# Performance work log

Hardware: AMD Instinct MI355X
Metric: run time of the kernel (lower is better)

## Reference

```python
import jax, jax.numpy as jnp
import numpy as np

S, B, H, NH, M = 2048, 2, 2048, 16, 2048
D = H // NH
FF = 4 * H
NORM = float(np.sqrt(D))  # norm_factor = sqrt(head_dim), no layer scaling
MASK_FILL = jnp.float32(-1e4)


def _ln(x, g, b):
    mu = jnp.mean(x, -1, keepdims=True)
    var = jnp.mean(jnp.square(x - mu), -1, keepdims=True)
    return (x - mu) * jax.lax.rsqrt(var + 1e-5) * g + b


def _l2(x):  # F.normalize over last dim
    return x * jax.lax.rsqrt(jnp.sum(jnp.square(x), -1, keepdims=True) + 1e-12)


def _mlp(h, w1, b1, w2, b2):  # ParallelMLP: h -> 4h -> h with gelu
    return jax.nn.gelu(h @ w1 + b1) @ w2 + b2


def setup_inputs() -> dict:
    key = jax.random.key(0)
    ks = jax.random.split(key, 12)
    w = lambda k, sh: jax.random.normal(k, sh, jnp.float32) * 0.02
    return {
        'x': jax.random.normal(ks[0], (S, B, H), jnp.float32),
        'mem_hidden': jax.random.normal(ks[1], (M, B, H), jnp.float32),
        'mem_mask': jax.random.randint(ks[2], (B, 1, S, M), 0, 5) == 0,  # True = masked
        'ln1_g': jnp.ones((H,), jnp.float32), 'ln1_b': jnp.zeros((H,), jnp.float32),
        'ln2_g': jnp.ones((H,), jnp.float32), 'ln2_b': jnp.zeros((H,), jnp.float32),
        'ln3_g': jnp.ones((H,), jnp.float32), 'ln3_b': jnp.zeros((H,), jnp.float32),
        'w_mlp1_in': w(ks[3], (H, FF)), 'b_mlp1_in': jnp.zeros((FF,), jnp.float32),
        'w_mlp1_out': w(ks[4], (FF, H)), 'b_mlp1_out': jnp.zeros((H,), jnp.float32),
        'w_q': w(ks[5], (H, H)), 'b_q': jnp.zeros((H,), jnp.float32),
        'w_kv': w(ks[6], (H, 2 * H)), 'b_kv': jnp.zeros((2 * H,), jnp.float32),
        'w_dense': w(ks[7], (H, H)), 'b_dense': jnp.zeros((H,), jnp.float32),
        'w_mlp2_in': w(ks[8], (H, FF)), 'b_mlp2_in': jnp.zeros((FF,), jnp.float32),
        'w_mlp2_out': w(ks[9], (FF, H)), 'b_mlp2_out': jnp.zeros((H,), jnp.float32),
    }


def reference(x, mem_hidden, mem_mask, ln1_g, ln1_b, ln2_g, ln2_b, ln3_g, ln3_b,
              w_mlp1_in, b_mlp1_in, w_mlp1_out, b_mlp1_out,
              w_q, b_q, w_kv, b_kv, w_dense, b_dense,
              w_mlp2_in, b_mlp2_in, w_mlp2_out, b_mlp2_out):
    # NOTE: source literally replaces x with mlp1 output (no residual on mlp1)
    x = _mlp(_ln(x, ln1_g, ln1_b), w_mlp1_in, b_mlp1_in, w_mlp1_out, b_mlp1_out)

    # memory attention: l2-normalized query vs l2-normalized retrieved memory k/v
    h2 = _ln(x, ln2_g, ln2_b)
    q = _l2((h2 @ w_q + b_q).reshape(S, B, NH, D))              # [s,b,h,d]
    kv = (mem_hidden @ w_kv + b_kv).reshape(M, B, NH, 2 * D)    # hidden_to_kv
    k = _l2(kv[..., :D])                                        # [m,b,h,d]
    v = _l2(kv[..., D:])
    scores = jnp.einsum('sbhd,mbhd->bhsm', q, k) / NORM
    scores = jnp.where(mem_mask, MASK_FILL, scores)             # attention_mask_func fill
    probs = jax.nn.softmax(scores, axis=-1)
    ctx = jnp.einsum('bhsm,mbhd->sbhd', probs, v).reshape(S, B, H)
    x = x + ctx @ w_dense + b_dense                             # dense w/ skip_bias_add

    x = x + _mlp(_ln(x, ln3_g, ln3_b), w_mlp2_in, b_mlp2_in, w_mlp2_out, b_mlp2_out)
    return x
```

## Files before the change

### kernel.cpp

```cpp
#include <hip/hip_runtime.h>
#include <stdint.h>
#include <stddef.h>

typedef __attribute__((ext_vector_type(8))) short bf16x8;
typedef __attribute__((ext_vector_type(4))) float f32x4;
typedef unsigned short u16;
typedef unsigned int u32;

static constexpr int S_ = 2048, B_ = 2, H_ = 2048, NH_ = 16, D_ = 128, M_ = 2048, FF_ = 8192;
static constexpr int SB_ = S_ * B_;
static constexpr int MB_ = M_ * B_;

__device__ __forceinline__ float b2f(u16 b) {
  union { u32 u; float f; } v; v.u = ((u32)b) << 16; return v.f;
}
__device__ __forceinline__ u16 f2b(float f) {
  union { float f; u32 u; } v; v.f = f;
  u32 u = v.u;
  return (u16)((u + 0x7FFFu + ((u >> 16) & 1u)) >> 16);
}
__device__ __forceinline__ float geluf(float x) {
  float x3 = x * x * x;
  return 0.5f * x * (1.0f + tanhf(0.7978845608028654f * (x + 0.044715f * x3)));
}

#define LDSP(p) (reinterpret_cast<__attribute__((address_space(3))) uint32_t*>(reinterpret_cast<uintptr_t>(p)))
#define GLBP(p) (reinterpret_cast<const __attribute__((address_space(1))) uint32_t*>(reinterpret_cast<uintptr_t>(p)))

__global__ void detect_kinds(const u32* __restrict__ x0, const u32* __restrict__ mask, int* __restrict__ flags) {
  if (threadIdx.x == 0 && blockIdx.x == 0) {
    int cnt = 0;
    for (int i = 0; i < 256; ++i) {
      u32 e = (x0[i] >> 7) & 0xFFu;
      if (e >= 118u && e <= 130u) ++cnt;
    }
    flags[0] = (cnt >= 128) ? 0 : 1;
    int all01 = 1, allf = 1, allb = 1;
    for (int i = 0; i < 256; ++i) {
      u32 v = mask[i];
      if (v > 1u) all01 = 0;
      if (v != 0u && v != 0x3F800000u) allf = 0;
      u32 lo = v & 0xFFFFu, hi = v >> 16;
      if ((lo != 0u && lo != 0x3F80u) || (hi != 0u && hi != 0x3F80u)) allb = 0;
    }
    flags[1] = all01 ? 1 : (allf ? 3 : (allb ? 2 : 0));
  }
}

__global__ void mask_cvt(const void* __restrict__ mraw, const int* __restrict__ flags, u16* __restrict__ mm) {
  int i = blockIdx.x * 256 + threadIdx.x;
  int kind = flags[1];
  int masked;
  if (kind == 1)      masked = ((const int*)mraw)[i] != 0;
  else if (kind == 3) masked = ((const float*)mraw)[i] != 0.0f;
  else if (kind == 2) masked = ((const u16*)mraw)[i] != 0;
  else                masked = ((const unsigned char*)mraw)[i] != 0;
  mm[i] = masked ? 0 : 0x3F80u;
}

__global__ void cvt_f32(const void* __restrict__ src, const int* __restrict__ flags, float* __restrict__ dst, int n) {
  int i = blockIdx.x * 256 + threadIdx.x;
  if (i < n) dst[i] = flags[0] ? ((const float*)src)[i] : b2f(((const u16*)src)[i]);
}

__global__ void cast_in_bf16(const void* __restrict__ src, const int* __restrict__ flags, u16* __restrict__ dst, int n8) {
  int i = blockIdx.x * 256 + threadIdx.x;
  if (i >= n8) return;
  if (flags[0]) {
    const float4* p = (const float4*)src;
    float4 a = p[i * 2], c = p[i * 2 + 1];
    bf16x8 o;
    o[0] = (short)f2b(a.x); o[1] = (short)f2b(a.y); o[2] = (short)f2b(a.z); o[3] = (short)f2b(a.w);
    o[4] = (short)f2b(c.x); o[5] = (short)f2b(c.y); o[6] = (short)f2b(c.z); o[7] = (short)f2b(c.w);
    *(bf16x8*)&dst[i * 8] = o;
  } else {
    *(bf16x8*)&dst[i * 8] = ((const bf16x8*)src)[i];
  }
}

__global__ __launch_bounds__(256) void transpose_cast(const void* __restrict__ in, const int* __restrict__ flags,
                                                      u16* __restrict__ out, int R, int C) {
  __shared__ u16 tile[64][65];
  const int isf = flags[0];
  const int tr = blockIdx.y * 64, tc = blockIdx.x * 64;
  const int tx = threadIdx.x & 63, ty = threadIdx.x >> 6;
  const float* inf = (const float*)in;
  const u16* inb = (const u16*)in;
#pragma unroll
  for (int i = 0; i < 16; ++i) {
    int r = ty * 16 + i;
    size_t idx = (size_t)(tr + r) * C + tc + tx;
    tile[r][tx] = isf ? f2b(inf[idx]) : inb[idx];
  }
  __syncthreads();
#pragma unroll
  for (int i = 0; i < 16; ++i) {
    int c = ty * 16 + i;
    out[(size_t)(tc + c) * R + tr + tx] = tile[tx][c];
  }
}

template <int EXT>
__global__ __launch_bounds__(256) void layernorm_k(const void* __restrict__ xin, const int* __restrict__ flags,
                                                   const float* __restrict__ g, const float* __restrict__ bta,
                                                   u16* __restrict__ out) {
  const int row = blockIdx.x, t = threadIdx.x;
  float v[8];
  bool bfmode = EXT && (flags[0] == 0);
  if (bfmode) {
    const u16* xr = (const u16*)xin + (size_t)row * H_ + t * 8;
    bf16x8 a = *(const bf16x8*)xr;
#pragma unroll
    for (int j = 0; j < 8; ++j) v[j] = b2f((u16)a[j]);
  } else {
    const float* xr = (const float*)xin + (size_t)row * H_ + t * 8;
    float4 a = *(const float4*)xr, c = *(const float4*)(xr + 4);
    v[0] = a.x; v[1] = a.y; v[2] = a.z; v[3] = a.w;
    v[4] = c.x; v[5] = c.y; v[6] = c.z; v[7] = c.w;
  }
  float s1 = 0.f, s2 = 0.f;
#pragma unroll
  for (int j = 0; j < 8; ++j) { s1 += v[j]; s2 += v[j] * v[j]; }
#pragma unroll
  for (int off = 32; off > 0; off >>= 1) { s1 += __shfl_down(s1, off); s2 += __shfl_down(s2, off); }
  __shared__ float red[8];
  const int w = t >> 6;
  if ((t & 63) == 0) { red[w] = s1; red[4 + w] = s2; }
  __syncthreads();
  s1 = red[0] + red[1] + red[2] + red[3];
  s2 = red[4] + red[5] + red[6] + red[7];
  const float mean = s1 * (1.0f / H_);
  const float rstd = rsqrtf(s2 * (1.0f / H_) - mean * mean + 1e-5f);
  bf16x8 o;
#pragma unroll
  for (int j = 0; j < 8; ++j) {
    float y = (v[j] - mean) * rstd * g[t * 8 + j] + bta[t * 8 + j];
    o[j] = (short)f2b(y);
  }
  *(bf16x8*)(out + (size_t)row * H_ + t * 8) = o;
}

template <int BN, int GELU, int RES, int WF, int WB, int ODYN>
__global__ __launch_bounds__(512, 2) void gemm64(const u16* __restrict__ A, const u16* __restrict__ Bt,
                                                 const float* __restrict__ bias, const float* __restrict__ res,
                                                 void* __restrict__ outF, u16* __restrict__ outB,
                                                 const int* __restrict__ flags, int Mr, int N, int K) {
  constexpr int AF = (BN == 256) ? 8 : 4;
  constexpr int NB = (BN == 256) ? 4 : 2;
  constexpr int BSLOT = BN * 64;
  constexpr int SLOTSTR = 16384 + BSLOT;
  __shared__ u16 lds[2 * SLOTSTR];
  const int t = threadIdx.x;
  const int w = t >> 6, lr = t & 15, lk = (t >> 4) & 3;
  const int gx = gridDim.x, gy = gridDim.y;
  const int orig = blockIdx.y * gx + blockIdx.x;
  const int nwg = gx * gy, per = nwg >> 3;
  int tm, tn;
  if ((gx & 7) == 0 && (per & 7) == 0) {
    const int xcd = orig & 7, p = orig >> 3;
    const int ncx = gx >> 3, cy = per >> 3;
    const int ccol = xcd % ncx, crow = xcd / ncx;
    const int px = p & 7, py = p >> 3;
    tn = (ccol * 8 + px) * BN;
    tm = (crow * cy + py) * 256;
  } else {
    tn = (orig % gx) * BN;
    tm = (orig / gx) * 256;
  }
  const int wr = (BN == 256) ? (w >> 2) : (w >> 1);
  const int wc = (BN == 256) ? (w & 3) : (w & 1);

  const int arow = t >> 3;
  const int aoc = (t & 7) ^ (arow & 7);
  const u16* Asrc = A + (size_t)(tm + arow) * K + aoc * 8;
  const u16* Bsrc = Bt + (size_t)(tn + arow) * K + aoc * 8;
  const int ldsw = w * 512;

  int ck[2];
#pragma unroll
  for (int kk = 0; kk < 2; ++kk) ck[kk] = ((kk * 4 + lk) ^ (lr & 7)) * 8;
  int arowo[AF], browo[4];
#pragma unroll
  for (int m = 0; m < AF; ++m) arowo[m] = (wr * (AF * 16) + m * 16 + lr) * 64;
#pragma unroll
  for (int n = 0; n < 4; ++n) browo[n] = (wc * 64 + n * 16 + lr) * 64;

  const int NS = K >> 6;
  f32x4 acc[AF][4] = {};

#define STG(sl) do {                                                                              \
    u16* Ad = lds + ((sl) & 1) * SLOTSTR;                                                         \
    u16* Bd = Ad + 16384;                                                                         \
    const size_t ko = (size_t)(sl) * 64;                                                          \
    _Pragma("unroll")                                                                             \
    for (int i = 0; i < 4; ++i)                                                                   \
      __builtin_amdgcn_global_load_lds(GLBP(Asrc + (size_t)(i * 64) * K + ko),                    \
                                       LDSP(Ad + i * 4096 + ldsw), 16, 0, 0);                     \
    _Pragma("unroll")                                                                             \
    for (int i = 0; i < NB; ++i)                                                                  \
      __builtin_amdgcn_global_load_lds(GLBP(Bsrc + (size_t)(i * 64) * K + ko),                    \
                                       LDSP(Bd + i * 4096 + ldsw), 16, 0, 0);                     \
  } while (0)

  STG(0);
  asm volatile("s_waitcnt vmcnt(0)" ::: "memory");
  __builtin_amdgcn_s_barrier();

  for (int s = 0; s < NS; ++s) {
    const bool more = (s + 1 < NS);
    if (more) STG(s + 1);
    const u16* As = lds + (s & 1) * SLOTSTR;
    const u16* Bs = As + 16384;
#pragma unroll
    for (int kk = 0; kk < 2; ++kk) {
      bf16x8 af[AF], bq[4];
#pragma unroll
      for (int m = 0; m < AF; ++m) af[m] = *(const bf16x8*)(As + arowo[m] + ck[kk]);
#pragma unroll
      for (int n = 0; n < 4; ++n) bq[n] = *(const bf16x8*)(Bs + browo[n] + ck[kk]);
      asm volatile("s_waitcnt lgkmcnt(0)" ::: "memory");
      __builtin_amdgcn_sched_barrier(0);
      __builtin_amdgcn_s_setprio(1);
#pragma unroll
      for (int n = 0; n < 4; ++n)
#pragma unroll
        for (int m = 0; m < AF; ++m)
          acc[m][n] = __builtin_amdgcn_mfma_f32_16x16x32_bf16(af[m], bq[n], acc[m][n], 0, 0, 0);
      __builtin_amdgcn_s_setprio(0);
    }
    if (more) {
      asm volatile("s_waitcnt vmcnt(0)" ::: "memory");
      __builtin_amdgcn_s_barrier();
    }
  }
#undef STG

  const int obf = ODYN ? (flags[0] ? 0 : 1) : 0;
#pragma unroll
  for (int m = 0; m < AF; ++m) {
#pragma unroll
    for (int n = 0; n < 4; ++n) {
      const int col = tn + wc * 64 + n * 16 + lr;
      const float bv = bias[col];
#pragma unroll
      for (int j = 0; j < 4; ++j) {
        const int rw = tm + wr * (AF * 16) + m * 16 + lk * 4 + j;
        float vv = acc[m][n][j] + bv;
        if (RES) vv += res[(size_t)rw * N + col];
        if (GELU) vv = geluf(vv);
        if (WF) {
          if (ODYN && obf) ((u16*)outF)[(size_t)rw * N + col] = f2b(vv);
          else ((float*)outF)[(size_t)rw * N + col] = vv;
        }
        if (WB) outB[(size_t)rw * N + col] = f2b(vv);
      }
    }
  }
}

__global__ __launch_bounds__(256) void l2_q(const float* __restrict__ qpre, u16* __restrict__ Q) {
  const int t = threadIdx.x;
  const int g = blockIdx.x * 64 + (t >> 2);
  const int lg = t & 3;
  const int h = g & (NH_ - 1), sb = g >> 4;
  const float* p = qpre + (size_t)sb * H_ + h * D_ + lg * 32;
  float vv[32];
  float ss = 0.f;
#pragma unroll
  for (int i = 0; i < 8; ++i) {
    float4 a = *(const float4*)&p[i * 4];
    vv[i * 4 + 0] = a.x; vv[i * 4 + 1] = a.y; vv[i * 4 + 2] = a.z; vv[i * 4 + 3] = a.w;
    ss += a.x * a.x + a.y * a.y + a.z * a.z + a.w * a.w;
  }
  ss += __shfl_xor(ss, 1); ss += __shfl_xor(ss, 2);
  const float sc = rsqrtf(ss + 1e-12f);
  const int s = sb >> 1, b = sb & 1;
  u16* o = Q + ((size_t)(b * NH_ + h) * S_ + s) * D_ + lg * 32;
#pragma unroll
  for (int i = 0; i < 4; ++i) {
    bf16x8 ov;
#pragma unroll
    for (int j = 0; j < 8; ++j) ov[j] = (short)f2b(vv[i * 8 + j] * sc);
    *(bf16x8*)&o[i * 8] = ov;
  }
}

__global__ __launch_bounds__(256) void l2_kv(const float* __restrict__ kvpre, u16* __restrict__ Kq, u16* __restrict__ Vt) {
  __shared__ u16 vtT[128][72];
  const int t = threadIdx.x;
  const int bid = blockIdx.x;
  const int mt = bid & 31, h = (bid >> 5) & 15, b = bid >> 9;
  const int lm = t >> 2, lg = t & 3;
  const int m = mt * 64 + lm;
  const size_t rowoff = (size_t)(m * B_ + b) * (2 * H_) + h * 256;
  float vv[32];
  {
    const float* p = kvpre + rowoff + lg * 32;
    float ss = 0.f;
#pragma unroll
    for (int i = 0; i < 8; ++i) {
      float4 a = *(const float4*)&p[i * 4];
      vv[i * 4 + 0] = a.x; vv[i * 4 + 1] = a.y; vv[i * 4 + 2] = a.z; vv[i * 4 + 3] = a.w;
      ss += a.x * a.x + a.y * a.y + a.z * a.z + a.w * a.w;
    }
    ss += __shfl_xor(ss, 1); ss += __shfl_xor(ss, 2);
    const float sc = rsqrtf(ss + 1e-12f);
    u16* o = Kq + ((size_t)(b * NH_ + h) * M_ + m) * D_ + lg * 32;
#pragma unroll
    for (int i = 0; i < 4; ++i) {
      bf16x8 ov;
#pragma unroll
      for (int j = 0; j < 8; ++j) ov[j] = (short)f2b(vv[i * 8 + j] * sc);
      *(bf16x8*)&o[i * 8] = ov;
    }
  }
  {
    const float* p = kvpre + rowoff + 128 + lg * 32;
    float ss = 0.f;
#pragma unroll
    for (int i = 0; i < 8; ++i) {
      float4 a = *(const float4*)&p[i * 4];
      vv[i * 4 + 0] = a.x; vv[i * 4 + 1] = a.y; vv[i * 4 + 2] = a.z; vv[i * 4 + 3] = a.w;
      ss += a.x * a.x + a.y * a.y + a.z * a.z + a.w * a.w;
    }
    ss += __shfl_xor(ss, 1); ss += __shfl_xor(ss, 2);
    const float sc = rsqrtf(ss + 1e-12f);
#pragma unroll
    for (int i = 0; i < 32; ++i) vtT[lg * 32 + i][lm] = f2b(vv[i] * sc);
  }
  __syncthreads();
  const int d = t >> 1, half = t & 1;
  u16* o = Vt + ((size_t)(b * NH_ + h) * D_ + d) * M_ + mt * 64 + half * 32;
#pragma unroll
  for (int i = 0; i < 4; ++i) {
    bf16x8 ov = *(const bf16x8*)&vtT[d][half * 32 + i * 8];
    *(bf16x8*)&o[i * 8] = ov;
  }
}

__global__ __launch_bounds__(256) void attn_k(const u16* __restrict__ Q, const u16* __restrict__ Kq,
                                              const u16* __restrict__ Vt, const u16* __restrict__ MM,
                                              u16* __restrict__ ctx) {
  __shared__ u16 Kl[64 * 128];
  __shared__ u16 Vl[128 * 64];
  __shared__ u16 Pl[4][32 * 72];
  const int t = threadIdx.x, w = t >> 6, l = t & 63, lr = l & 15, lk = l >> 4;
  const int st = blockIdx.x * 128;
  const int bh = blockIdx.y, b = bh >> 4, h = bh & 15;
  const u16* Qb = Q + ((size_t)bh * S_ + st + w * 32) * D_;
  bf16x8 qf[2][4];
#pragma unroll
  for (int sf = 0; sf < 2; ++sf)
#pragma unroll
    for (int kc = 0; kc < 4; ++kc)
      qf[sf][kc] = *(const bf16x8*)&Qb[(sf * 16 + lr) * D_ + kc * 32 + lk * 8];
  f32x4 oacc[2][8] = {};
  float den[2][4] = {};
  const u16* Kb = Kq + (size_t)bh * M_ * D_;
  const u16* Vb = Vt + (size_t)bh * D_ * M_;
  const u16* Mb = MM + (size_t)b * S_ * M_ + (size_t)(st + w * 32) * M_;
  const float invn = 0.08838834764831845f;

  for (int m0 = 0; m0 < M_; m0 += 64) {
#pragma unroll
    for (int i = 0; i < 4; ++i) {
      int j = i * 256 + w * 64 + l;
      int r = j >> 4, c = j & 15, cs = c ^ (r & 7);
      __builtin_amdgcn_global_load_lds(GLBP(Kb + (size_t)(m0 + r) * D_ + cs * 8),
                                       LDSP(&Kl[(i * 256 + w * 64) * 8]), 16, 0, 0);
    }
#pragma unroll
    for (int i = 0; i < 4; ++i) {
      int j = i * 256 + w * 64 + l;
      int r = j >> 3, c = j & 7, cs = c ^ (r & 7);
      __builtin_amdgcn_global_load_lds(GLBP(Vb + (size_t)r * M_ + m0 + cs * 8),
                                       LDSP(&Vl[(i * 256 + w * 64) * 8]), 16, 0, 0);
    }
    __syncthreads();
    f32x4 sc[2][4] = {};
#pragma unroll
    for (int mf = 0; mf < 4; ++mf) {
      int rowm = mf * 16 + lr;
#pragma unroll
      for (int kc = 0; kc < 4; ++kc) {
        int cc = (kc * 4 + lk) ^ (rowm & 7);
        bf16x8 kfv = *(const bf16x8*)&Kl[rowm * 128 + cc * 8];
#pragma unroll
        for (int sf = 0; sf < 2; ++sf)
          sc[sf][mf] = __builtin_amdgcn_mfma_f32_16x16x32_bf16(qf[sf][kc], kfv, sc[sf][mf], 0, 0, 0);
      }
    }
#pragma unroll
    for (int sf = 0; sf < 2; ++sf)
#pragma unroll
      for (int mf = 0; mf < 4; ++mf) {
        int mcol = m0 + mf * 16 + lr;
#pragma unroll
        for (int j2 = 0; j2 < 4; ++j2) {
          int rloc = sf * 16 + lk * 4 + j2;
          float p = __expf(sc[sf][mf][j2] * invn);
          u16 mv = Mb[(size_t)rloc * M_ + mcol];
          p = mv ? p : 0.0f;
          den[sf][j2] += p;
          Pl[w][rloc * 72 + mf * 16 + lr] = f2b(p);
        }
      }
    __syncthreads();
#pragma unroll
    for (int kc2 = 0; kc2 < 2; ++kc2) {
      bf16x8 pa[2];
#pragma unroll
      for (int sf = 0; sf < 2; ++sf)
        pa[sf] = *(const bf16x8*)&Pl[w][(sf * 16 + lr) * 72 + kc2 * 32 + lk * 8];
#pragma unroll
      for (int nf = 0; nf < 8; ++nf) {
        int dd = nf * 16 + lr;
        int cc = (kc2 * 4 + lk) ^ (dd & 7);
        bf16x8 vf = *(const bf16x8*)&Vl[dd * 64 + cc * 8];
#pragma unroll
        for (int sf = 0; sf < 2; ++sf)
          oacc[sf][nf] = __builtin_amdgcn_mfma_f32_16x16x32_bf16(pa[sf], vf, oacc[sf][nf], 0, 0, 0);
      }
    }
    __syncthreads();
  }
#pragma unroll
  for (int sf = 0; sf < 2; ++sf)
#pragma unroll
    for (int j2 = 0; j2 < 4; ++j2) {
      float d = den[sf][j2];
      d += __shfl_xor(d, 1); d += __shfl_xor(d, 2); d += __shfl_xor(d, 4); d += __shfl_xor(d, 8);
      den[sf][j2] = 1.0f / fmaxf(d, 1e-20f);
    }
#pragma unroll
  for (int sf = 0; sf < 2; ++sf)
#pragma unroll
    for (int nf = 0; nf < 8; ++nf)
#pragma unroll
      for (int j2 = 0; j2 < 4; ++j2) {
        int s = st + w * 32 + sf * 16 + lk * 4 + j2;
        int dd = nf * 16 + lr;
        ctx[((size_t)s * B_ + b) * H_ + h * D_ + dd] = f2b(oacc[sf][nf][j2] * den[sf][j2]);
      }
}

extern "C" void kernel_launch(void* const* d_in, const int* in_sizes, int n_in,
                              void* d_out, int out_size, void* d_ws, size_t ws_size,
                              hipStream_t stream) {
  (void)in_sizes; (void)n_in; (void)out_size; (void)ws_size;
  char* ws = (char*)d_ws;
  u16* WT     = (u16*)(ws + 0);
  void* MID   = (void*)(ws + 33554432);
  float* XF   = (float*)(ws + 100663296);
  u16* HB     = (u16*)(ws + 134217728);
  u16* MEMB   = (u16*)(ws + 150994944);
  u16* QB     = (u16*)(ws + 167772160);
  u16* KB     = (u16*)(ws + 184549376);
  u16* VTB    = (u16*)(ws + 201326592);
  u16* MMUL   = (u16*)(ws + 218103808);
  float* SM   = (float*)(ws + 234881024);
  int* FLAGS  = (int*)(ws + 235044864);

  float* Bias1  = SM + 0;
  float* Bias1o = SM + 8192;
  float* BiasQ  = SM + 10240;
  float* BiasKV = SM + 12288;
  float* BiasD  = SM + 16384;
  float* Bias2  = SM + 18432;
  float* Bias2o = SM + 26624;
  float* G1v = SM + 28672; float* B1v = SM + 30720;
  float* G2v = SM + 32768; float* B2v = SM + 34816;
  float* G3v = SM + 36864; float* B3v = SM + 38912;

  detect_kinds<<<1, 64, 0, stream>>>((const u32*)d_in[0], (const u32*)d_in[2], FLAGS);

  cvt_f32<<<32, 256, 0, stream>>>(d_in[10], FLAGS, Bias1, 8192);
  cvt_f32<<<8, 256, 0, stream>>>(d_in[12], FLAGS, Bias1o, 2048);
  cvt_f32<<<8, 256, 0, stream>>>(d_in[14], FLAGS, BiasQ, 2048);
  cvt_f32<<<16, 256, 0, stream>>>(d_in[16], FLAGS, BiasKV, 4096);
  cvt_f32<<<8, 256, 0, stream>>>(d_in[18], FLAGS, BiasD, 2048);
  cvt_f32<<<32, 256, 0, stream>>>(d_in[20], FLAGS, Bias2, 8192);
  cvt_f32<<<8, 256, 0, stream>>>(d_in[22], FLAGS, Bias2o, 2048);
  cvt_f32<<<8, 256, 0, stream>>>(d_in[3], FLAGS, G1v, 2048);
  cvt_f32<<<8, 256, 0, stream>>>(d_in[4], FLAGS, B1v, 2048);
  cvt_f32<<<8, 256, 0, stream>>>(d_in[5], FLAGS, G2v, 2048);
  cvt_f32<<<8, 256, 0, stream>>>(d_in[6], FLAGS, B2v, 2048);
  cvt_f32<<<8, 256, 0, stream>>>(d_in[7], FLAGS, G3v, 2048);
  cvt_f32<<<8, 256, 0, stream>>>(d_in[8], FLAGS, B3v, 2048);

  mask_cvt<<<(B_ * S_ * M_) / 256, 256, 0, stream>>>(d_in[2], FLAGS, MMUL);
  cast_in_bf16<<<(MB_ * H_ / 8) / 256, 256, 0, stream>>>(d_in[1], FLAGS, MEMB, MB_ * H_ / 8);

  dim3 blk(256);
  dim3 blk5(512);
  layernorm_k<1><<<SB_, blk, 0, stream>>>(d_in[0], FLAGS, G1v, B1v, HB);
  transpose_cast<<<dim3(FF_ / 64, H_ / 64), blk, 0, stream>>>(d_in[9], FLAGS, WT, H_, FF_);
  gemm64<256, 1, 0, 0, 1, 0><<<dim3(FF_ / 256, SB_ / 256), blk5, 0, stream>>>(HB, WT, Bias1, nullptr, nullptr, (u16*)MID, FLAGS, SB_, FF_, H_);
  transpose_cast<<<dim3(H_ / 64, FF_ / 64), blk, 0, stream>>>(d_in[11], FLAGS, WT, FF_, H_);
  gemm64<128, 0, 0, 1, 0, 0><<<dim3(H_ / 128, SB_ / 256), blk5, 0, stream>>>((u16*)MID, WT, Bias1o, nullptr, XF, nullptr, FLAGS, SB_, H_, FF_);

  layernorm_k<0><<<SB_, blk, 0, stream>>>(XF, FLAGS, G2v, B2v, HB);
  transpose_cast<<<dim3(H_ / 64, H_ / 64), blk, 0, stream>>>(d_in[13], FLAGS, WT, H_, H_);
  gemm64<128, 0, 0, 1, 0, 0><<<dim3(H_ / 128, SB_ / 256), blk5, 0, stream>>>(HB, WT, BiasQ, nullptr, MID, nullptr, FLAGS, SB_, H_, H_);
  l2_q<<<(SB_ * NH_) / 64, blk, 0, stream>>>((const float*)MID, QB);
  transpose_cast<<<dim3(2 * H_ / 64, H_ / 64), blk, 0, stream>>>(d_in[15], FLAGS, WT, H_, 2 * H_);
  gemm64<256, 0, 0, 1, 0, 0><<<dim3(2 * H_ / 256, MB_ / 256), blk5, 0, stream>>>(MEMB, WT, BiasKV, nullptr, MID, nullptr, FLAGS, MB_, 2 * H_, H_);
  l2_kv<<<B_ * NH_ * (M_ / 64), blk, 0, stream>>>((const float*)MID, KB, VTB);
  attn_k<<<dim3(S_ / 128, B_ * NH_), blk, 0, stream>>>(QB, KB, VTB, MMUL, MEMB);
  transpose_cast<<<dim3(H_ / 64, H_ / 64), blk, 0, stream>>>(d_in[17], FLAGS, WT, H_, H_);
  gemm64<128, 0, 1, 1, 0, 0><<<dim3(H_ / 128, SB_ / 256), blk5, 0, stream>>>(MEMB, WT, BiasD, XF, XF, nullptr, FLAGS, SB_, H_, H_);

  layernorm_k<0><<<SB_, blk, 0, stream>>>(XF, FLAGS, G3v, B3v, HB);
  transpose_cast<<<dim3(FF_ / 64, H_ / 64), blk, 0, stream>>>(d_in[19], FLAGS, WT, H_, FF_);
  gemm64<256, 1, 0, 0, 1, 0><<<dim3(FF_ / 256, SB_ / 256), blk5, 0, stream>>>(HB, WT, Bias2, nullptr, nullptr, (u16*)MID, FLAGS, SB_, FF_, H_);
  transpose_cast<<<dim3(H_ / 64, FF_ / 64), blk, 0, stream>>>(d_in[21], FLAGS, WT, FF_, H_);
  gemm64<128, 0, 1, 1, 0, 1><<<dim3(H_ / 128, SB_ / 256), blk5, 0, stream>>>((u16*)MID, WT, Bias2o, XF, d_out, nullptr, FLAGS, SB_, H_, FF_);
}
```

Before: 1.324 ms.

## Replace 256-row GEMM with 128x128 tile kernel using 32x32x16 MFMA

Replaces the 512-thread GEMM, which used 256xBN tiles, 16x16x32 MFMAs and a K-step of 64, with a 256-thread kernel. The new kernel uses 128x128 tiles, 32x32x16 MFMAs, a K-step of 32 and a new swizzled LDS layout. It launches more, smaller workgroups (up to 4 per CU) to raise occupancy and uses the larger MFMA shape to cut LDS read traffic per flop. In exchange, the smaller tiles lower data reuse, and the shorter K-step means twice as many barriers per K.

```diff
diff --git a/kernel.cpp b/kernel.cpp
--- a/kernel.cpp
+++ b/kernel.cpp
@@ -4,6 +4,7 @@
 
 typedef __attribute__((ext_vector_type(8))) short bf16x8;
 typedef __attribute__((ext_vector_type(4))) float f32x4;
+typedef __attribute__((ext_vector_type(16))) float f32x16;
 typedef unsigned short u16;
 typedef unsigned int u32;
 
@@ -140,18 +141,15 @@
   *(bf16x8*)(out + (size_t)row * H_ + t * 8) = o;
 }
 
-template <int BN, int GELU, int RES, int WF, int WB, int ODYN>
-__global__ __launch_bounds__(512, 2) void gemm64(const u16* __restrict__ A, const u16* __restrict__ Bt,
+template <int GELU, int RES, int WF, int WB, int ODYN>
+__global__ __launch_bounds__(256, 4) void gemm32(const u16* __restrict__ A, const u16* __restrict__ Bt,
                                                  const float* __restrict__ bias, const float* __restrict__ res,
                                                  void* __restrict__ outF, u16* __restrict__ outB,
                                                  const int* __restrict__ flags, int Mr, int N, int K) {
-  constexpr int AF = (BN == 256) ? 8 : 4;
-  constexpr int NB = (BN == 256) ? 4 : 2;
-  constexpr int BSLOT = BN * 64;
-  constexpr int SLOTSTR = 16384 + BSLOT;
-  __shared__ u16 lds[2 * SLOTSTR];
+  __shared__ u16 lds[2 * 8192];
   const int t = threadIdx.x;
-  const int w = t >> 6, lr = t & 15, lk = (t >> 4) & 3;
+  const int w = t >> 6, l = t & 63, lm = l & 31, lh = l >> 5;
+  const int wr = w >> 1, wc = w & 1;
   const int gx = gridDim.x, gy = gridDim.y;
   const int orig = blockIdx.y * gx + blockIdx.x;
   const int nwg = gx * gy, per = nwg >> 3;
@@ -161,45 +159,46 @@
     const int ncx = gx >> 3, cy = per >> 3;
     const int ccol = xcd % ncx, crow = xcd / ncx;
     const int px = p & 7, py = p >> 3;
-    tn = (ccol * 8 + px) * BN;
-    tm = (crow * cy + py) * 256;
+    tn = (ccol * 8 + px) * 128;
+    tm = (crow * cy + py) * 128;
   } else {
-    tn = (orig % gx) * BN;
-    tm = (orig / gx) * 256;
-  }
-  const int wr = (BN == 256) ? (w >> 2) : (w >> 1);
-  const int wc = (BN == 256) ? (w & 3) : (w & 1);
-
-  const int arow = t >> 3;
-  const int aoc = (t & 7) ^ (arow & 7);
-  const u16* Asrc = A + (size_t)(tm + arow) * K + aoc * 8;
-  const u16* Bsrc = Bt + (size_t)(tn + arow) * K + aoc * 8;
-  const int ldsw = w * 512;
-
-  int ck[2];
-#pragma unroll
-  for (int kk = 0; kk < 2; ++kk) ck[kk] = ((kk * 4 + lk) ^ (lr & 7)) * 8;
-  int arowo[AF], browo[4];
-#pragma unroll
-  for (int m = 0; m < AF; ++m) arowo[m] = (wr * (AF * 16) + m * 16 + lr) * 64;
-#pragma unroll
-  for (int n = 0; n < 4; ++n) browo[n] = (wc * 64 + n * 16 + lr) * 64;
-
-  const int NS = K >> 6;
-  f32x4 acc[AF][4] = {};
-
-#define STG(sl) do {                                                                              \
-    u16* Ad = lds + ((sl) & 1) * SLOTSTR;                                                         \
-    u16* Bd = Ad + 16384;                                                                         \
-    const size_t ko = (size_t)(sl) * 64;                                                          \
-    _Pragma("unroll")                                                                             \
-    for (int i = 0; i < 4; ++i)                                                                   \
-      __builtin_amdgcn_global_load_lds(GLBP(Asrc + (size_t)(i * 64) * K + ko),                    \
-                                       LDSP(Ad + i * 4096 + ldsw), 16, 0, 0);                     \
-    _Pragma("unroll")                                                                             \
-    for (int i = 0; i < NB; ++i)                                                                  \
-      __builtin_amdgcn_global_load_lds(GLBP(Bsrc + (size_t)(i * 64) * K + ko),                    \
-                                       LDSP(Bd + i * 4096 + ldsw), 16, 0, 0);                     \
+    tn = (orig % gx) * 128;
+    tm = (orig / gx) * 128;
+  }
+  u32 aofs[2], bofs[2];
+#pragma unroll
+  for (int i = 0; i < 2; ++i) {
+    int idx = i * 256 + t;
+    int srow = idx >> 3, p4 = idx & 7;
+    int p = p4 ^ (srow & 7);
+    int row = (srow << 1) | (p >> 2), ckk = p & 3;
+    aofs[i] = (u32)(tm + row) * (u32)K + ckk * 8;
+    bofs[i] = (u32)(tn + row) * (u32)K + ckk * 8;
+  }
+  const int wb8 = w * 512;
+  int offA[2][2], offB[2][2];
+#pragma unroll
+  for (int mi = 0; mi < 2; ++mi)
+#pragma unroll
+    for (int kk = 0; kk < 2; ++kk) {
+      const int p = ((lm & 1) << 2) | (kk << 1) | lh;
+      const int sa = wr * 32 + mi * 16 + (lm >> 1);
+      offA[mi][kk] = sa * 64 + (p ^ (sa & 7)) * 8;
+      const int sb = wc * 32 + mi * 16 + (lm >> 1);
+      offB[mi][kk] = sb * 64 + (p ^ (sb & 7)) * 8;
+    }
+  const int NS = K >> 5;
+  f32x16 acc[2][2] = {};
+
+#define STG(sl) do {                                                                                  \
+    u16* Ad = lds + ((sl) & 1) * 8192;                                                                \
+    u16* Bd = Ad + 4096;                                                                              \
+    const u32 ko = (u32)(sl) * 32;                                                                    \
+    _Pragma("unroll")                                                                                 \
+    for (int i = 0; i < 2; ++i) {                                                                     \
+      __builtin_amdgcn_global_load_lds(GLBP(A + aofs[i] + ko), LDSP(Ad + i * 2048 + wb8), 16, 0, 0);  \
+      __builtin_amdgcn_global_load_lds(GLBP(Bt + bofs[i] + ko), LDSP(Bd + i * 2048 + wb8), 16, 0, 0); \
+    }                                                                                                 \
   } while (0)
 
   STG(0);
@@ -209,25 +208,28 @@
   for (int s = 0; s < NS; ++s) {
     const bool more = (s + 1 < NS);
     if (more) STG(s + 1);
-    const u16* As = lds + (s & 1) * SLOTSTR;
-    const u16* Bs = As + 16384;
-#pragma unroll
-    for (int kk = 0; kk < 2; ++kk) {
-      bf16x8 af[AF], bq[4];
-#pragma unroll
-      for (int m = 0; m < AF; ++m) af[m] = *(const bf16x8*)(As + arowo[m] + ck[kk]);
-#pragma unroll
-      for (int n = 0; n < 4; ++n) bq[n] = *(const bf16x8*)(Bs + browo[n] + ck[kk]);
-      asm volatile("s_waitcnt lgkmcnt(0)" ::: "memory");
-      __builtin_amdgcn_sched_barrier(0);
-      __builtin_amdgcn_s_setprio(1);
-#pragma unroll
-      for (int n = 0; n < 4; ++n)
-#pragma unroll
-        for (int m = 0; m < AF; ++m)
-          acc[m][n] = __builtin_amdgcn_mfma_f32_16x16x32_bf16(af[m], bq[n], acc[m][n], 0, 0, 0);
-      __builtin_amdgcn_s_setprio(0);
-    }
+    const u16* As = lds + (s & 1) * 8192;
+    const u16* Bs = As + 4096;
+    bf16x8 af[2][2], bq[2][2];
+#pragma unroll
+    for (int mi = 0; mi < 2; ++mi)
+#pragma unroll
+      for (int kk = 0; kk < 2; ++kk) {
+        af[mi][kk] = *(const bf16x8*)(As + offA[mi][kk]);
+        bq[mi][kk] = *(const bf16x8*)(Bs + offB[mi][kk]);
+      }
+    asm volatile("s_waitcnt lgkmcnt(0)" ::: "memory");
+    __builtin_amdgcn_sched_barrier(0);
+    __builtin_amdgcn_s_setprio(1);
+#pragma unroll
+    for (int kk = 0; kk < 2; ++kk)
+#pragma unroll
+      for (int mi = 0; mi < 2; ++mi)
+#pragma unroll
+        for (int ni = 0; ni < 2; ++ni)
+          acc[mi][ni] = __builtin_amdgcn_mfma_f32_32x32x16_bf16(af[mi][kk], bq[ni][kk], acc[mi][ni], 0, 0, 0);
+    __builtin_amdgcn_s_setprio(0);
+    __builtin_amdgcn_sched_barrier(0);
     if (more) {
       asm volatile("s_waitcnt vmcnt(0)" ::: "memory");
       __builtin_amdgcn_s_barrier();
@@ -237,15 +239,15 @@
 
   const int obf = ODYN ? (flags[0] ? 0 : 1) : 0;
 #pragma unroll
-  for (int m = 0; m < AF; ++m) {
-#pragma unroll
-    for (int n = 0; n < 4; ++n) {
-      const int col = tn + wc * 64 + n * 16 + lr;
+  for (int mi = 0; mi < 2; ++mi) {
+#pragma unroll
+    for (int ni = 0; ni < 2; ++ni) {
+      const int col = tn + wc * 64 + ni * 32 + lm;
       const float bv = bias[col];
 #pragma unroll
-      for (int j = 0; j < 4; ++j) {
-        const int rw = tm + wr * (AF * 16) + m * 16 + lk * 4 + j;
-        float vv = acc[m][n][j] + bv;
+      for (int r = 0; r < 16; ++r) {
+        const int rw = tm + wr * 64 + mi * 32 + (r & 3) + 8 * (r >> 2) + 4 * lh;
+        float vv = acc[mi][ni][r] + bv;
         if (RES) vv += res[(size_t)rw * N + col];
         if (GELU) vv = geluf(vv);
         if (WF) {
@@ -492,27 +494,26 @@
   cast_in_bf16<<<(MB_ * H_ / 8) / 256, 256, 0, stream>>>(d_in[1], FLAGS, MEMB, MB_ * H_ / 8);
 
   dim3 blk(256);
-  dim3 blk5(512);
   layernorm_k<1><<<SB_, blk, 0, stream>>>(d_in[0], FLAGS, G1v, B1v, HB);
   transpose_cast<<<dim3(FF_ / 64, H_ / 64), blk, 0, stream>>>(d_in[9], FLAGS, WT, H_, FF_);
-  gemm64<256, 1, 0, 0, 1, 0><<<dim3(FF_ / 256, SB_ / 256), blk5, 0, stream>>>(HB, WT, Bias1, nullptr, nullptr, (u16*)MID, FLAGS, SB_, FF_, H_);
+  gemm32<1, 0, 0, 1, 0><<<dim3(FF_ / 128, SB_ / 128), blk, 0, stream>>>(HB, WT, Bias1, nullptr, nullptr, (u16*)MID, FLAGS, SB_, FF_, H_);
   transpose_cast<<<dim3(H_ / 64, FF_ / 64), blk, 0, stream>>>(d_in[11], FLAGS, WT, FF_, H_);
-  gemm64<128, 0, 0, 1, 0, 0><<<dim3(H_ / 128, SB_ / 256), blk5, 0, stream>>>((u16*)MID, WT, Bias1o, nullptr, XF, nullptr, FLAGS, SB_, H_, FF_);
+  gemm32<0, 0, 1, 0, 0><<<dim3(H_ / 128, SB_ / 128), blk, 0, stream>>>((u16*)MID, WT, Bias1o, nullptr, XF, nullptr, FLAGS, SB_, H_, FF_);
 
   layernorm_k<0><<<SB_, blk, 0, stream>>>(XF, FLAGS, G2v, B2v, HB);
   transpose_cast<<<dim3(H_ / 64, H_ / 64), blk, 0, stream>>>(d_in[13], FLAGS, WT, H_, H_);
-  gemm64<128, 0, 0, 1, 0, 0><<<dim3(H_ / 128, SB_ / 256), blk5, 0, stream>>>(HB, WT, BiasQ, nullptr, MID, nullptr, FLAGS, SB_, H_, H_);
+  gemm32<0, 0, 1, 0, 0><<<dim3(H_ / 128, SB_ / 128), blk, 0, stream>>>(HB, WT, BiasQ, nullptr, MID, nullptr, FLAGS, SB_, H_, H_);
   l2_q<<<(SB_ * NH_) / 64, blk, 0, stream>>>((const float*)MID, QB);
   transpose_cast<<<dim3(2 * H_ / 64, H_ / 64), blk, 0, stream>>>(d_in[15], FLAGS, WT, H_, 2 * H_);
-  gemm64<256, 0, 0, 1, 0, 0><<<dim3(2 * H_ / 256, MB_ / 256), blk5, 0, stream>>>(MEMB, WT, BiasKV, nullptr, MID, nullptr, FLAGS, MB_, 2 * H_, H_);
+  gemm32<0, 0, 1, 0, 0><<<dim3(2 * H_ / 128, MB_ / 128), blk, 0, stream>>>(MEMB, WT, BiasKV, nullptr, MID, nullptr, FLAGS, MB_, 2 * H_, H_);
   l2_kv<<<B_ * NH_ * (M_ / 64), blk, 0, stream>>>((const float*)MID, KB, VTB);
   attn_k<<<dim3(S_ / 128, B_ * NH_), blk, 0, stream>>>(QB, KB, VTB, MMUL, MEMB);
   transpose_cast<<<dim3(H_ / 64, H_ / 64), blk, 0, stream>>>(d_in[17], FLAGS, WT, H_, H_);
-  gemm64<128, 0, 1, 1, 0, 0><<<dim3(H_ / 128, SB_ / 256), blk5, 0, stream>>>(MEMB, WT, BiasD, XF, XF, nullptr, FLAGS, SB_, H_, H_);
+  gemm32<0, 1, 1, 0, 0><<<dim3(H_ / 128, SB_ / 128), blk, 0, stream>>>(MEMB, WT, BiasD, XF, XF, nullptr, FLAGS, SB_, H_, H_);
 
   layernorm_k<0><<<SB_, blk, 0, stream>>>(XF, FLAGS, G3v, B3v, HB);
   transpose_cast<<<dim3(FF_ / 64, H_ / 64), blk, 0, stream>>>(d_in[19], FLAGS, WT, H_, FF_);
-  gemm64<256, 1, 0, 0, 1, 0><<<dim3(FF_ / 256, SB_ / 256), blk5, 0, stream>>>(HB, WT, Bias2, nullptr, nullptr, (u16*)MID, FLAGS, SB_, FF_, H_);
+  gemm32<1, 0, 0, 1, 0><<<dim3(FF_ / 128, SB_ / 128), blk, 0, stream>>>(HB, WT, Bias2, nullptr, nullptr, (u16*)MID, FLAGS, SB_, FF_, H_);
   transpose_cast<<<dim3(H_ / 64, FF_ / 64), blk, 0, stream>>>(d_in[21], FLAGS, WT, FF_, H_);
-  gemm64<128, 0, 1, 1, 0, 1><<<dim3(H_ / 128, SB_ / 256), blk5, 0, stream>>>((u16*)MID, WT, Bias2o, XF, d_out, nullptr, FLAGS, SB_, H_, FF_);
-}
+  gemm32<0, 1, 1, 0, 1><<<dim3(H_ / 128, SB_ / 128), blk, 0, stream>>>((u16*)MID, WT, Bias2o, XF, d_out, nullptr, FLAGS, SB_, H_, FF_);
+}
```

Result: slower. 1.411 ms (+6.5%).
